# Kernel optimization log

Hardware: AMD Instinct MI355X
Metric: run time of the kernel (lower is better)

Reference implementation:

```python
import jax, jax.numpy as jnp
import numpy as np

H, W = 256, 256
BACKGROUND = 1.0


def setup_inputs() -> dict:
    key = jax.random.key(0)
    k1, k2, k3, k4, k5 = jax.random.split(key, 5)
    N = 1024
    # means inside the camera frustum: z in [2,6], x/z,y/z in [-0.8,0.8]
    z = jax.random.uniform(k1, (N,), minval=2.0, maxval=6.0)
    xy = jax.random.uniform(k2, (N, 2), minval=-0.8, maxval=0.8) * z[:, None]
    means = jnp.concatenate([xy, z[:, None]], axis=-1).astype(jnp.float32)
    colors = jax.random.uniform(k3, (N, 3), dtype=jnp.float32)
    opacity = jax.random.uniform(k4, (N,), dtype=jnp.float32)
    scales = jax.random.uniform(k5, (N, 1), dtype=jnp.float32) * 0.1 + 0.01
    fx = fy = float(W)
    intrinsics = jnp.array([[fx, 0.0, W / 2.0],
                            [0.0, fy, H / 2.0],
                            [0.0, 0.0, 1.0]], dtype=jnp.float32)
    world_to_camera = jnp.eye(4, dtype=jnp.float32)
    return {"means": means, "colors": colors, "opacity": opacity,
            "scales": scales, "intrinsics": intrinsics,
            "world_to_camera": world_to_camera}


def reference(means, colors, opacity, scales, intrinsics, world_to_camera):
    N = means.shape[0]
    # project points: p_cam = (W2C @ [p;1])[:3]; uv = (K @ p_cam)[:2] / z
    ph = jnp.concatenate([means, jnp.ones((N, 1), means.dtype)], axis=-1)
    p_cam = (ph @ world_to_camera.T)[:, :3]          # [N,3]
    z = p_cam[:, 2]                                   # [N]
    proj = p_cam @ intrinsics.T                       # [N,3]
    uv = proj[:, :2] / z[:, None]                     # [N,2]

    # validity mask (replaces data-dependent boolean indexing; invalid -> alpha 0)
    valid = ((z > 1e-4)
             & (uv[:, 0] >= -W) & (uv[:, 0] <= 2 * W)
             & (uv[:, 1] >= -H) & (uv[:, 1] <= 2 * H))
    op = jnp.where(valid, opacity, 0.0)

    yy, xx = jnp.meshgrid(jnp.arange(H, dtype=means.dtype),
                          jnp.arange(W, dtype=means.dtype), indexing="ij")
    grid = jnp.stack([xx, yy], axis=-1)               # [H,W,2]

    diff = grid[None] - uv[:, None, None, :]          # [N,H,W,2]
    sigma = jnp.maximum(scales[:, 0] * max(H, W), 1.0)[:, None, None]
    alpha = op[:, None, None] * jnp.exp(-0.5 * jnp.sum(diff * diff, axis=-1)
                                        / (sigma * sigma))   # [N,H,W]
    alpha = jnp.clip(alpha, 0.0, 0.95)

    alpha_sum = jnp.sum(alpha, axis=0)                # [H,W]
    weights = alpha / (alpha_sum[None] + 1e-6)        # [N,H,W]
    accum = jnp.clip(alpha_sum, 0.0, 1.0)             # [H,W]

    rgb = jnp.einsum("nhw,nc->chw", weights, colors)  # [3,H,W]
    rgb = rgb * accum[None] + BACKGROUND * (1.0 - accum[None])
    depth = jnp.einsum("nhw,n->hw", weights, z)[None]  # [1,H,W]
    return jnp.clip(rgb, 0.0, 1.0), accum[None], depth
```

## Files before the change

### kernel.cpp

```cpp
#include <hip/hip_runtime.h>
#include <math.h>

#define HH 256
#define WW 256
#define NTHREADS 256
#define CHUNKG 1024
#define NROUND (CHUNKG / NTHREADS)
#define BPX 128
#define HWPIX (HH * WW)
#define ECUT (-9.5f)

typedef short s8v __attribute__((ext_vector_type(8)));
typedef float f4v __attribute__((ext_vector_type(4)));

__device__ __forceinline__ unsigned pk_trunc(float lo, float hi) {
    return (__float_as_uint(hi) & 0xFFFF0000u) | (__float_as_uint(lo) >> 16);
}
__device__ __forceinline__ short bf16h(float v) {
    return (short)(__float_as_uint(v) >> 16);
}
__device__ __forceinline__ float fexp2(float x) {
    return __builtin_amdgcn_exp2f(x);
}

__global__ __launch_bounds__(NTHREADS) void render_kernel(
    const float* __restrict__ means,
    const float* __restrict__ colors,
    const float* __restrict__ opacity,
    const float* __restrict__ scales,
    const float* __restrict__ K,
    const float* __restrict__ M,
    float* __restrict__ out,
    int N)
{
    __shared__ float    prm3[CHUNKG * 3];
    __shared__ unsigned bfr[(CHUNKG / 32) * 256];
    __shared__ int      scnt[4 * NROUND];
    __shared__ float    esum[5 * BPX];

    short* bfr16 = (short*)bfr;

    const int tid  = threadIdx.x;
    const int lane = tid & 63;
    const int wv   = tid >> 6;
    const int y    = blockIdx.x >> 1;
    const int x0   = (blockIdx.x & 1) * BPX;
    const float yf  = (float)y;
    const float x0f = (float)x0;
    const int kq   = (lane >> 4) << 3;

    for (int e = tid; e < (CHUNKG / 32) * 256; e += NTHREADS) bfr[e] = 0;

    f4v acc[2];
    acc[0] = (f4v){0.f, 0.f, 0.f, 0.f};
    acc[1] = (f4v){0.f, 0.f, 0.f, 0.f};

    float xs[2], xxs[2];
    #pragma unroll
    for (int t = 0; t < 2; ++t) {
        xs[t]  = (float)(x0 + wv * 32 + t * 16 + (lane & 15));
        xxs[t] = xs[t] * xs[t];
    }

    for (int base = 0; base < N; base += CHUNKG) {
        __syncthreads();

        float Ar[NROUND], Br[NROUND], Er[NROUND];
        float4 cfr[NROUND];
        bool  keepr[NROUND];
        int   prer[NROUND];

        #pragma unroll
        for (int r = 0; r < NROUND; ++r) {
            const int n = base + r * NTHREADS + tid;
            float A = 0.f, Bc = 0.f, E = -INFINITY;
            float4 cf = make_float4(0.f, 0.f, 0.f, 0.f);
            float blkpeak = -INFINITY;
            if (n < N) {
                const float wx = means[3 * n + 0];
                const float wy = means[3 * n + 1];
                const float wz = means[3 * n + 2];
                const float px = M[0] * wx + M[1] * wy + M[2]  * wz + M[3];
                const float py = M[4] * wx + M[5] * wy + M[6]  * wz + M[7];
                const float pz = M[8] * wx + M[9] * wy + M[10] * wz + M[11];
                const float rz = 1.0f / pz;
                const float u  = (K[0] * px + K[1] * py + K[2] * pz) * rz;
                const float v  = (K[4] * py + K[5] * pz) * rz;
                const bool valid = (pz > 1e-4f)
                                && (u >= -(float)WW) && (u <= 2.0f * (float)WW)
                                && (v >= -(float)HH) && (v <= 2.0f * (float)HH);
                if (valid) {
                    const float op  = opacity[n];
                    const float sig = fmaxf(scales[n] * 256.0f, 1.0f);
                    const float coef = -0.72134752044448170368f / (sig * sig);
                    const float lop = __log2f(op);
                    const float dyv = yf - v;
                    const float xc  = fminf(fmaxf(u, x0f), x0f + (float)(BPX - 1));
                    const float dxc = xc - u;
                    blkpeak = fmaf(coef, fmaf(dxc, dxc, dyv * dyv), lop);
                    A  = coef;
                    Bc = -2.0f * coef * u;
                    const float C = -2.0f * coef * v;
                    const float D = fmaf(coef, fmaf(u, u, v * v), lop);
                    E  = fmaf(fmaf(A, yf, C), yf, D);
                    cf = make_float4(colors[3 * n + 0], colors[3 * n + 1],
                                     colors[3 * n + 2], pz);
                }
            }
            const bool keep = (blkpeak > ECUT);
            const unsigned long long mask = __ballot(keep);
            if (lane == 0) scnt[r * 4 + wv] = __popcll(mask);
            Ar[r] = A; Br[r] = Bc; Er[r] = E; cfr[r] = cf;
            keepr[r] = keep;
            prer[r] = __popcll(mask & ((1ull << lane) - 1ull));
        }
        __syncthreads();

        int rbase[NROUND];
        int running = 0;
        #pragma unroll
        for (int r = 0; r < NROUND; ++r) {
            int b = running;
            #pragma unroll
            for (int w = 0; w < 4; ++w) {
                if (w < wv) b += scnt[r * 4 + w];
                running += scnt[r * 4 + w];
            }
            rbase[r] = b;
        }
        const int cnt    = running;
        const int padded = (cnt + 31) & ~31;
        const int nch    = padded >> 5;

        #pragma unroll
        for (int r = 0; r < NROUND; ++r) {
            if (keepr[r]) {
                const int pos = rbase[r] + prer[r];
                prm3[3 * pos + 0] = Ar[r];
                prm3[3 * pos + 1] = Br[r];
                prm3[3 * pos + 2] = Er[r];
                const int chunk = pos >> 5;
                const int k     = pos & 31;
                const int eb    = chunk * 256 + (k >> 3) * 64 + ((k & 7) >> 1);
                const int par   = k & 1;
                bfr16[(eb +  0) * 2 + par] = (short)0x3F80;
                bfr16[(eb +  4) * 2 + par] = bf16h(cfr[r].x);
                bfr16[(eb +  8) * 2 + par] = bf16h(cfr[r].y);
                bfr16[(eb + 12) * 2 + par] = bf16h(cfr[r].z);
                bfr16[(eb + 16) * 2 + par] = bf16h(cfr[r].w);
            }
        }
        if (tid < padded - cnt) {
            const int pos = cnt + tid;
            prm3[3 * pos + 0] = 0.f;
            prm3[3 * pos + 1] = 0.f;
            prm3[3 * pos + 2] = -INFINITY;
        }
        __syncthreads();

        __builtin_amdgcn_s_setprio(1);
        const float4* prm4 = (const float4*)prm3;
        #pragma unroll 2
        for (int c = 0; c < nch; ++c) {
            const int qb = 24 * c + 6 * (kq >> 3);
            float4 q0 = prm4[qb + 0], q1 = prm4[qb + 1], q2 = prm4[qb + 2];
            float4 q3 = prm4[qb + 3], q4 = prm4[qb + 4], q5 = prm4[qb + 5];
            const float Ag[8] = {q0.x, q0.w, q1.z, q2.y, q3.x, q3.w, q4.z, q5.y};
            const float Bg[8] = {q0.y, q1.x, q1.w, q2.z, q3.y, q4.x, q4.w, q5.z};
            const float Eg[8] = {q0.z, q1.y, q2.x, q2.w, q3.z, q4.y, q5.x, q5.w};

            union { s8v v; uint4 q; } Bf;
            Bf.q = *(const uint4*)&bfr[c * 256 + lane * 4];

            #pragma unroll
            for (int t = 0; t < 2; ++t) {
                union { s8v v; unsigned u[4]; } Af;
                #pragma unroll
                for (int r = 0; r < 4; ++r) {
                    const float a0 = fminf(fexp2(fmaf(Bg[2*r],   xs[t], fmaf(Ag[2*r],   xxs[t], Eg[2*r]))),   0.95f);
                    const float a1 = fminf(fexp2(fmaf(Bg[2*r+1], xs[t], fmaf(Ag[2*r+1], xxs[t], Eg[2*r+1]))), 0.95f);
                    Af.u[r] = pk_trunc(a0, a1);
                }
                acc[t] = __builtin_amdgcn_mfma_f32_16x16x32_bf16(Af.v, Bf.v, acc[t], 0, 0, 0);
            }
        }
        __builtin_amdgcn_s_setprio(0);
    }

    __syncthreads();
    const int col = lane & 15;
    if (col < 5) {
        const int rb = (lane >> 4) << 2;
        #pragma unroll
        for (int t = 0; t < 2; ++t) {
            #pragma unroll
            for (int r = 0; r < 4; ++r) {
                esum[col * BPX + wv * 32 + t * 16 + rb + r] = acc[t][r];
            }
        }
    }
    __syncthreads();

    if (tid < BPX) {
        const float s  = esum[0 * BPX + tid];
        const float ar = esum[1 * BPX + tid];
        const float ag = esum[2 * BPX + tid];
        const float ab = esum[3 * BPX + tid];
        const float az = esum[4 * BPX + tid];
        const float inv   = 1.0f / (s + 1e-6f);
        const float accum = fminf(s, 1.0f);
        const float bg    = 1.0f - accum;
        float* o = out + (size_t)y * WW + x0 + tid;
        o[0 * HWPIX] = fminf(fmaxf(fmaf(ar * inv, accum, bg), 0.0f), 1.0f);
        o[1 * HWPIX] = fminf(fmaxf(fmaf(ag * inv, accum, bg), 0.0f), 1.0f);
        o[2 * HWPIX] = fminf(fmaxf(fmaf(ab * inv, accum, bg), 0.0f), 1.0f);
        o[3 * HWPIX] = accum;
        o[4 * HWPIX] = az * inv;
    }
}

extern "C" void kernel_launch(void* const* d_in, const int* in_sizes, int n_in,
                              void* d_out, int out_size, void* d_ws, size_t ws_size,
                              hipStream_t stream) {
    const float* means      = (const float*)d_in[0];
    const float* colors     = (const float*)d_in[1];
    const float* opacity    = (const float*)d_in[2];
    const float* scales     = (const float*)d_in[3];
    const float* intrinsics = (const float*)d_in[4];
    const float* w2c        = (const float*)d_in[5];
    float* out = (float*)d_out;

    const int N = in_sizes[0] / 3;

    render_kernel<<<HH * 2, NTHREADS, 0, stream>>>(
        means, colors, opacity, scales, intrinsics, w2c, out, N);
}
```

Before: 12.09 us.

## Halve pixels per block and stage culled gaussians through a capped LDS buffer

Measured after the change: 12.30 us. About the same (+1.8%).

```diff
diff --git a/kernel.cpp b/kernel.cpp
--- a/kernel.cpp
+++ b/kernel.cpp
@@ -6,7 +6,9 @@
 #define NTHREADS 256
 #define CHUNKG 1024
 #define NROUND (CHUNKG / NTHREADS)
-#define BPX 128
+#define BPX 64
+#define CAP 256
+#define NCHCAP (CAP / 32)
 #define HWPIX (HH * WW)
 #define ECUT (-9.5f)
 
@@ -33,8 +35,8 @@
     float* __restrict__ out,
     int N)
 {
-    __shared__ float    prm3[CHUNKG * 3];
-    __shared__ unsigned bfr[(CHUNKG / 32) * 256];
+    __shared__ float    prm3[CAP * 3];
+    __shared__ unsigned bfr[NCHCAP * 256];
     __shared__ int      scnt[4 * NROUND];
     __shared__ float    esum[5 * BPX];
 
@@ -43,24 +45,17 @@
     const int tid  = threadIdx.x;
     const int lane = tid & 63;
     const int wv   = tid >> 6;
-    const int y    = blockIdx.x >> 1;
-    const int x0   = (blockIdx.x & 1) * BPX;
+    const int y    = blockIdx.x >> 2;
+    const int x0   = (blockIdx.x & 3) * BPX;
     const float yf  = (float)y;
     const float x0f = (float)x0;
     const int kq   = (lane >> 4) << 3;
 
-    for (int e = tid; e < (CHUNKG / 32) * 256; e += NTHREADS) bfr[e] = 0;
-
-    f4v acc[2];
-    acc[0] = (f4v){0.f, 0.f, 0.f, 0.f};
-    acc[1] = (f4v){0.f, 0.f, 0.f, 0.f};
-
-    float xs[2], xxs[2];
-    #pragma unroll
-    for (int t = 0; t < 2; ++t) {
-        xs[t]  = (float)(x0 + wv * 32 + t * 16 + (lane & 15));
-        xxs[t] = xs[t] * xs[t];
-    }
+    for (int e = tid; e < NCHCAP * 256; e += NTHREADS) bfr[e] = 0;
+
+    f4v acc = (f4v){0.f, 0.f, 0.f, 0.f};
+    const float xsv  = (float)(x0 + wv * 16 + (lane & 15));
+    const float xxsv = xsv * xsv;
 
     for (int base = 0; base < N; base += CHUNKG) {
         __syncthreads();
@@ -128,63 +123,67 @@
             }
             rbase[r] = b;
         }
-        const int cnt    = running;
-        const int padded = (cnt + 31) & ~31;
-        const int nch    = padded >> 5;
-
-        #pragma unroll
-        for (int r = 0; r < NROUND; ++r) {
-            if (keepr[r]) {
-                const int pos = rbase[r] + prer[r];
-                prm3[3 * pos + 0] = Ar[r];
-                prm3[3 * pos + 1] = Br[r];
-                prm3[3 * pos + 2] = Er[r];
-                const int chunk = pos >> 5;
-                const int k     = pos & 31;
-                const int eb    = chunk * 256 + (k >> 3) * 64 + ((k & 7) >> 1);
-                const int par   = k & 1;
-                bfr16[(eb +  0) * 2 + par] = (short)0x3F80;
-                bfr16[(eb +  4) * 2 + par] = bf16h(cfr[r].x);
-                bfr16[(eb +  8) * 2 + par] = bf16h(cfr[r].y);
-                bfr16[(eb + 12) * 2 + par] = bf16h(cfr[r].z);
-                bfr16[(eb + 16) * 2 + par] = bf16h(cfr[r].w);
-            }
-        }
-        if (tid < padded - cnt) {
-            const int pos = cnt + tid;
-            prm3[3 * pos + 0] = 0.f;
-            prm3[3 * pos + 1] = 0.f;
-            prm3[3 * pos + 2] = -INFINITY;
-        }
-        __syncthreads();
-
-        __builtin_amdgcn_s_setprio(1);
-        const float4* prm4 = (const float4*)prm3;
-        #pragma unroll 2
-        for (int c = 0; c < nch; ++c) {
-            const int qb = 24 * c + 6 * (kq >> 3);
-            float4 q0 = prm4[qb + 0], q1 = prm4[qb + 1], q2 = prm4[qb + 2];
-            float4 q3 = prm4[qb + 3], q4 = prm4[qb + 4], q5 = prm4[qb + 5];
-            const float Ag[8] = {q0.x, q0.w, q1.z, q2.y, q3.x, q3.w, q4.z, q5.y};
-            const float Bg[8] = {q0.y, q1.x, q1.w, q2.z, q3.y, q4.x, q4.w, q5.z};
-            const float Eg[8] = {q0.z, q1.y, q2.x, q2.w, q3.z, q4.y, q5.x, q5.w};
-
-            union { s8v v; uint4 q; } Bf;
-            Bf.q = *(const uint4*)&bfr[c * 256 + lane * 4];
+        const int cnt = running;
+
+        for (int s0 = 0; s0 < cnt; s0 += CAP) {
+            const int bc   = min(cnt - s0, CAP);
+            const int bpad = (bc + 31) & ~31;
+            const int nch  = bpad >> 5;
 
             #pragma unroll
-            for (int t = 0; t < 2; ++t) {
+            for (int r = 0; r < NROUND; ++r) {
+                if (keepr[r]) {
+                    const int pos = rbase[r] + prer[r] - s0;
+                    if (pos >= 0 && pos < CAP) {
+                        prm3[3 * pos + 0] = Ar[r];
+                        prm3[3 * pos + 1] = Br[r];
+                        prm3[3 * pos + 2] = Er[r];
+                        const int chunk = pos >> 5;
+                        const int k     = pos & 31;
+                        const int eb    = chunk * 256 + (k >> 3) * 64 + ((k & 7) >> 1);
+                        const int par   = k & 1;
+                        bfr16[(eb +  0) * 2 + par] = (short)0x3F80;
+                        bfr16[(eb +  4) * 2 + par] = bf16h(cfr[r].x);
+                        bfr16[(eb +  8) * 2 + par] = bf16h(cfr[r].y);
+                        bfr16[(eb + 12) * 2 + par] = bf16h(cfr[r].z);
+                        bfr16[(eb + 16) * 2 + par] = bf16h(cfr[r].w);
+                    }
+                }
+            }
+            if (tid < bpad - bc) {
+                const int pos = bc + tid;
+                prm3[3 * pos + 0] = 0.f;
+                prm3[3 * pos + 1] = 0.f;
+                prm3[3 * pos + 2] = -INFINITY;
+            }
+            __syncthreads();
+
+            __builtin_amdgcn_s_setprio(1);
+            const float4* prm4 = (const float4*)prm3;
+            #pragma unroll 2
+            for (int c = 0; c < nch; ++c) {
+                const int qb = 24 * c + 6 * (kq >> 3);
+                float4 q0 = prm4[qb + 0], q1 = prm4[qb + 1], q2 = prm4[qb + 2];
+                float4 q3 = prm4[qb + 3], q4 = prm4[qb + 4], q5 = prm4[qb + 5];
+                const float Ag[8] = {q0.x, q0.w, q1.z, q2.y, q3.x, q3.w, q4.z, q5.y};
+                const float Bg[8] = {q0.y, q1.x, q1.w, q2.z, q3.y, q4.x, q4.w, q5.z};
+                const float Eg[8] = {q0.z, q1.y, q2.x, q2.w, q3.z, q4.y, q5.x, q5.w};
+
+                union { s8v v; uint4 q; } Bf;
+                Bf.q = *(const uint4*)&bfr[c * 256 + lane * 4];
+
                 union { s8v v; unsigned u[4]; } Af;
                 #pragma unroll
                 for (int r = 0; r < 4; ++r) {
-                    const float a0 = fminf(fexp2(fmaf(Bg[2*r],   xs[t], fmaf(Ag[2*r],   xxs[t], Eg[2*r]))),   0.95f);
-                    const float a1 = fminf(fexp2(fmaf(Bg[2*r+1], xs[t], fmaf(Ag[2*r+1], xxs[t], Eg[2*r+1]))), 0.95f);
+                    const float a0 = fminf(fexp2(fmaf(Bg[2*r],   xsv, fmaf(Ag[2*r],   xxsv, Eg[2*r]))),   0.95f);
+                    const float a1 = fminf(fexp2(fmaf(Bg[2*r+1], xsv, fmaf(Ag[2*r+1], xxsv, Eg[2*r+1]))), 0.95f);
                     Af.u[r] = pk_trunc(a0, a1);
                 }
-                acc[t] = __builtin_amdgcn_mfma_f32_16x16x32_bf16(Af.v, Bf.v, acc[t], 0, 0, 0);
-            }
-        }
-        __builtin_amdgcn_s_setprio(0);
+                acc = __builtin_amdgcn_mfma_f32_16x16x32_bf16(Af.v, Bf.v, acc, 0, 0, 0);
+            }
+            __builtin_amdgcn_s_setprio(0);
+            __syncthreads();
+        }
     }
 
     __syncthreads();
@@ -192,11 +191,8 @@
     if (col < 5) {
         const int rb = (lane >> 4) << 2;
         #pragma unroll
-        for (int t = 0; t < 2; ++t) {
-            #pragma unroll
-            for (int r = 0; r < 4; ++r) {
-                esum[col * BPX + wv * 32 + t * 16 + rb + r] = acc[t][r];
-            }
+        for (int r = 0; r < 4; ++r) {
+            esum[col * BPX + wv * 16 + rb + r] = acc[r];
         }
     }
     __syncthreads();
@@ -232,6 +228,6 @@
 
     const int N = in_sizes[0] / 3;
 
-    render_kernel<<<HH * 2, NTHREADS, 0, stream>>>(
+    render_kernel<<<HH * 4, NTHREADS, 0, stream>>>(
         means, colors, opacity, scales, intrinsics, w2c, out, N);
 }
```
